# Kernel tuning notes

Measured on AMD Instinct MI355X. Metric: run time of the kernel, lower is better.

The kernel has to match this reference:

```python
import jax, jax.numpy as jnp
import numpy as np

H, W = 64, 64
B, P, F = 8, 512, 512
EXPAND = 0.02      # bbox expansion for soft silhouette (NDC units), DIB-R default
MULT = 1000.0      # DIB-R coordinate multiplier
DELTA = 7000.0     # soft prob falloff in multiplier-scaled squared units, DIB-R default
EPS = 1e-10


def setup_inputs() -> dict:
    key = jax.random.key(0)
    k1, k2, k3 = jax.random.split(key, 3)
    verts = 0.5 * jax.random.normal(k1, (B, P, 3), dtype=jnp.float32)
    faces = jax.random.randint(k2, (B, F, 3), 0, P, dtype=jnp.int32)
    colors = jax.random.uniform(k3, (B, P, 3), dtype=jnp.float32)
    camera_rot = jnp.tile(jnp.eye(3, dtype=jnp.float32)[None], (B, 1, 1))
    camera_pos = jnp.tile(jnp.array([0.0, 0.0, 3.0], dtype=jnp.float32)[None], (B, 1))
    fov_factor = 2.7475  # 1 / tan(fovy/2), fovy ~ 0.7 rad, aspect 1
    camera_proj = jnp.array([[fov_factor], [fov_factor], [-1.0]], dtype=jnp.float32)
    return {"verts": verts, "faces": faces, "camera_rot": camera_rot,
            "camera_pos": camera_pos, "camera_proj": camera_proj, "colors": colors}


def _render_one(verts_p3, faces_f3, rot_33, pos_3, proj_31, colors_p3):
    # --- perspective_projection (pixel2mesh convention: p' = rot^T (p - pos)) ---
    pcam = (verts_p3 - pos_3[None, :]) @ rot_33.T                 # [P,3] camera frame
    xy3 = pcam * proj_31.reshape(3)[None, :]
    xy = xy3[:, :2] / xy3[:, 2:3]                                  # [P,2] NDC
    tri3d = pcam[faces_f3]                                         # [F,3,3]
    tri2d = xy[faces_f3]                                           # [F,3,2]
    normal = jnp.cross(tri3d[:, 1] - tri3d[:, 0], tri3d[:, 2] - tri3d[:, 0])  # [F,3]
    normalz = normal[:, 2]
    normal1 = normal / (jnp.linalg.norm(normal, axis=1, keepdims=True) + 1e-12)
    # per-face vertex colors + hard-mask channel -> [F,3,4] (== color_1xfx12)
    cmask = jnp.ones((faces_f3.shape[0], 3, 1), dtype=colors_p3.dtype)
    cfeat = jnp.concatenate([colors_p3[faces_f3], cmask], axis=2)

    # --- linear_rasterizer: pixel grid in NDC ---
    xs = (2.0 * jnp.arange(W, dtype=jnp.float32) + 1.0 - W) / W
    ys = (H - 2.0 * jnp.arange(H, dtype=jnp.float32) - 1.0) / H
    x0 = xs[None, :, None]                                         # [1,W,1]
    y0 = ys[:, None, None]                                         # [H,1,1]
    ax, ay = tri2d[:, 0, 0], tri2d[:, 0, 1]
    bx, by = tri2d[:, 1, 0], tri2d[:, 1, 1]
    cx, cy = tri2d[:, 2, 0], tri2d[:, 2, 1]
    det = (by - cy) * (ax - cx) + (cx - bx) * (ay - cy)            # [F]
    det_safe = jnp.where(jnp.abs(det) < EPS, EPS, det)
    w0 = ((by - cy) * (x0 - cx) + (cx - bx) * (y0 - cy)) / det_safe  # [H,W,F]
    w1 = ((cy - ay) * (x0 - cx) + (ax - cx) * (y0 - cy)) / det_safe
    w2 = 1.0 - w0 - w1
    z = w0 * tri3d[:, 0, 2] + w1 * tri3d[:, 1, 2] + w2 * tri3d[:, 2, 2]  # [H,W,F]
    covered = (w0 >= 0) & (w1 >= 0) & (w2 >= 0)
    valid = covered & (normalz > 0) & (jnp.abs(det) > EPS)
    # hard z-buffer: camera looks along -z, so nearest face has max z
    zbuf = jnp.where(valid, z, -1e10)
    best = jnp.argmax(zbuf, axis=-1)                               # [H,W]
    anyv = jnp.any(valid, axis=-1)
    gw = lambda w: jnp.take_along_axis(w, best[..., None], axis=-1)[..., 0]
    g0, g1, g2 = gw(w0), gw(w1), gw(w2)
    cb = cfeat[best]                                               # [H,W,3,4]
    feat = (g0[..., None] * cb[..., 0, :] + g1[..., None] * cb[..., 1, :]
            + g2[..., None] * cb[..., 2, :])
    imfeat = jnp.where(anyv[..., None], feat, 0.0)                 # [H,W,4]

    # --- soft silhouette probability ---
    def seg_d2(px, py, qx, qy):
        vx, vy = qx - px, qy - py
        t = jnp.clip(((x0 - px) * vx + (y0 - py) * vy)
                     / (vx * vx + vy * vy + 1e-12), 0.0, 1.0)
        dx, dy = x0 - (px + t * vx), y0 - (py + t * vy)
        return dx * dx + dy * dy
    d2 = jnp.minimum(jnp.minimum(seg_d2(ax, ay, bx, by), seg_d2(bx, by, cx, cy)),
                     seg_d2(cx, cy, ax, ay))
    d2 = jnp.where(covered, 0.0, d2)                               # inside -> 0
    xmin = jnp.minimum(jnp.minimum(ax, bx), cx) - EXPAND
    xmax = jnp.maximum(jnp.maximum(ax, bx), cx) + EXPAND
    ymin = jnp.minimum(jnp.minimum(ay, by), cy) - EXPAND
    ymax = jnp.maximum(jnp.maximum(ay, by), cy) + EXPAND
    in_bbox = (x0 >= xmin) & (x0 <= xmax) & (y0 >= ymin) & (y0 <= ymax)
    contrib = jnp.where(in_bbox, jnp.exp(-d2 * (MULT * MULT) / DELTA), 0.0)
    improb = 1.0 - jnp.prod(1.0 - contrib, axis=-1, keepdims=True)  # [H,W,1]
    return imfeat, improb, normal1


def reference(verts, faces, camera_rot, camera_pos, camera_proj, colors):
    imfeat, improb, normal1 = jax.vmap(_render_one, in_axes=(0, 0, 0, 0, None, 0))(
        verts, faces, camera_rot, camera_pos, camera_proj, colors)
    imrender = imfeat[..., :3]     # [B,H,W,3]
    hardmask = imfeat[..., 3:]     # [B,H,W,1]
    return imrender, improb, normal1, hardmask
```

## Files before the change

### kernel.cpp

```cpp
#include <hip/hip_runtime.h>
#include <math.h>

#define NB 8
#define NP 512
#define NF 512
#define NH 64
#define NW 64
#define FEXPAND 0.02f
#define FEPS 1e-10f

#define IMG_OFF 0
#define PROB_OFF (NB*NH*NW*3)
#define NRM_OFF  (PROB_OFF + NB*NH*NW)
#define MASK_OFF (NRM_OFF + NB*NF*3)

__device__ __forceinline__ void bary(float e0x, float e0y, float e1x, float e1y,
                                     float det_safe, float cx, float cy,
                                     float x, float y,
                                     float& w0, float& w1, float& w2,
                                     float& dxc, float& dyc) {
  dxc = x - cx; dyc = y - cy;
  float n0 = __fadd_rn(__fmul_rn(e0x, dxc), __fmul_rn(e0y, dyc));
  float n1 = __fadd_rn(__fmul_rn(e1x, dxc), __fmul_rn(e1y, dyc));
  w0 = __fdiv_rn(n0, det_safe);
  w1 = __fdiv_rn(n1, det_safe);
  w2 = __fsub_rn(__fsub_rn(1.0f, w0), w1);
}

__global__ __launch_bounds__(1024, 8) void render_all(
    const float* __restrict__ verts, const int* __restrict__ faces,
    const float* __restrict__ rot, const float* __restrict__ pos,
    const float* __restrict__ proj, const float* __restrict__ colors,
    float* __restrict__ out)
{
  __shared__ __align__(16) float smem[NF*20];
  int tid  = threadIdx.x;
  int b    = blockIdx.x >> 6;
  int tile = blockIdx.x & 63;
  int wave = tid >> 6;
  int lane = tid & 63;
  int ix = (tile & 7)*8 + (lane & 7);
  int iy = (tile >> 3)*8 + (lane >> 3);
  float x = (2.0f*ix + 1.0f - 64.0f) * (1.0f/64.0f);
  float y = (64.0f - 2.0f*iy - 1.0f) * (1.0f/64.0f);

  if (tid < NF) {
    int t = b * NF + tid;
    float p0 = proj[0], p1 = proj[1], p2 = proj[2];
    float R0=rot[b*9+0],R1=rot[b*9+1],R2=rot[b*9+2];
    float R3=rot[b*9+3],R4=rot[b*9+4],R5=rot[b*9+5];
    float R6=rot[b*9+6],R7=rot[b*9+7],R8=rot[b*9+8];
    float ppx=pos[b*3+0], ppy=pos[b*3+1], ppz=pos[b*3+2];
    int idxs[3] = { faces[t*3+0], faces[t*3+1], faces[t*3+2] };
    float X[3],Y[3],Z[3],SX[3],SY[3];
#pragma unroll
    for (int k = 0; k < 3; ++k) {
      const float* v = verts + ((size_t)b*NP + idxs[k])*3;
      float dx = v[0]-ppx, dy = v[1]-ppy, dz = v[2]-ppz;
      float pcx = __fadd_rn(__fadd_rn(__fmul_rn(R0,dx),__fmul_rn(R1,dy)),__fmul_rn(R2,dz));
      float pcy = __fadd_rn(__fadd_rn(__fmul_rn(R3,dx),__fmul_rn(R4,dy)),__fmul_rn(R5,dz));
      float pcz = __fadd_rn(__fadd_rn(__fmul_rn(R6,dx),__fmul_rn(R7,dy)),__fmul_rn(R8,dz));
      X[k]=pcx; Y[k]=pcy; Z[k]=pcz;
      float dn = __fmul_rn(pcz, p2);
      SX[k] = __fdiv_rn(__fmul_rn(pcx, p0), dn);
      SY[k] = __fdiv_rn(__fmul_rn(pcy, p1), dn);
    }
    float e1x=X[1]-X[0], e1y=Y[1]-Y[0], e1z=Z[1]-Z[0];
    float e2x=X[2]-X[0], e2y=Y[2]-Y[0], e2z=Z[2]-Z[0];
    float nzel = __fsub_rn(__fmul_rn(e1x,e2y), __fmul_rn(e1y,e2x));
    if (tile == 0) {
      float m0 = __fmul_rn(e1z, e2y); float nxf = __fmaf_rn(e1y, e2z, -m0);
      float m1 = __fmul_rn(e1x, e2z); float nyf = __fmaf_rn(e1z, e2x, -m1);
      float m2 = __fmul_rn(e1y, e2x); float nzf = __fmaf_rn(e1x, e2y, -m2);
      float nn = __fsqrt_rn(__fadd_rn(__fadd_rn(__fmul_rn(nxf,nxf),__fmul_rn(nyf,nyf)),
                                      __fmul_rn(nzf,nzf)));
      float den = __fadd_rn(nn, 1e-12f);
      out[NRM_OFF + (size_t)t*3+0] = __fdiv_rn(nxf, den);
      out[NRM_OFF + (size_t)t*3+1] = __fdiv_rn(nyf, den);
      out[NRM_OFF + (size_t)t*3+2] = __fdiv_rn(nzf, den);
    }
    float ax=SX[0],ay=SY[0],bx=SX[1],by=SY[1],cx=SX[2],cy=SY[2];
    float det = __fadd_rn(__fmul_rn(__fsub_rn(by,cy),__fsub_rn(ax,cx)),
                          __fmul_rn(__fsub_rn(cx,bx),__fsub_rn(ay,cy)));
    float det_safe = (fabsf(det) < FEPS) ? FEPS : det;
    float validf = ((nzel > 0.0f) && (fabsf(det) > FEPS)) ? 1.0f : 0.0f;
    float* d = &smem[tid*20];
    d[0]=ax; d[1]=ay; d[2]=bx; d[3]=by;
    d[4]=cx; d[5]=cy; d[6]=det_safe; d[7]=validf;
    d[8]=Z[0]; d[9]=Z[1]; d[10]=Z[2];
    float vx=bx-ax, vy=by-ay;
    d[11]=1.0f/(vx*vx+vy*vy+1e-12f);
    d[12]=fminf(fminf(ax,bx),cx)-FEXPAND; d[13]=fmaxf(fmaxf(ax,bx),cx)+FEXPAND;
    d[14]=fminf(fminf(ay,by),cy)-FEXPAND; d[15]=fmaxf(fmaxf(ay,by),cy)+FEXPAND;
    vx=cx-bx; vy=cy-by;
    d[16]=1.0f/(vx*vx+vy*vy+1e-12f);
    vx=ax-cx; vy=ay-cy;
    d[17]=1.0f/(vx*vx+vy*vy+1e-12f);
    d[18]=0.0f; d[19]=0.0f;
  }
  __syncthreads();

  float bestz = -1e10f;
  int   bestf = 0;
  float bw0 = 0.0f, bw1 = 0.0f, bw2 = 0.0f;
  float prod  = 1.0f;

  float4 bb = *(const float4*)&smem[wave*20 + 12];
  for (int j = 0; j < 32; ++j) {
    int f = (j << 4) + wave;
    float4 bbn = bb;
    if (j < 31) bbn = *(const float4*)&smem[(f + 16)*20 + 12];
    bool inb = (x >= bb.x) && (x <= bb.y) && (y >= bb.z) && (y <= bb.w);
    if (__any(inb)) {
      const float* r = &smem[f*20];
      float4 q0 = *(const float4*)(r);
      float4 q1 = *(const float4*)(r + 4);
      float4 q2 = *(const float4*)(r + 8);
      float iBC = r[16], iCA = r[17];
      float ax=q0.x, ay=q0.y, bxx=q0.z, byy=q0.w, cx=q1.x, cy=q1.y;
      float e0x=__fsub_rn(byy,cy), e0y=__fsub_rn(cx,bxx);
      float e1x=__fsub_rn(cy,ay),  e1y=__fsub_rn(ax,cx);
      float w0,w1,w2,dxc,dyc;
      bary(e0x,e0y,e1x,e1y, q1.z, cx, cy, x, y, w0,w1,w2,dxc,dyc);
      bool covered = (w0 >= 0.0f) && (w1 >= 0.0f) && (w2 >= 0.0f);
      bool valid   = covered && (q1.w > 0.5f);
      float z = __fadd_rn(__fadd_rn(__fmul_rn(w0,q2.x), __fmul_rn(w1,q2.y)),
                          __fmul_rn(w2,q2.z));
      if (inb) {
        float zval = valid ? z : -1e10f;
        if (zval > bestz) { bestz = zval; bestf = f; bw0 = w0; bw1 = w1; bw2 = w2; }
        float dxa = x - ax, dya = y - ay;
        float vABx=__fsub_rn(bxx,ax), vABy=__fsub_rn(byy,ay);
        float t1 = fminf(fmaxf((dxa*vABx + dya*vABy)*q2.w, 0.0f), 1.0f);
        float rx = dxa - t1*vABx, ry = dya - t1*vABy;
        float d2 = rx*rx + ry*ry;
        float dxb = x - bxx, dyb = y - byy;
        float vBCx=__fsub_rn(cx,bxx), vBCy=__fsub_rn(cy,byy);
        t1 = fminf(fmaxf((dxb*vBCx + dyb*vBCy)*iBC, 0.0f), 1.0f);
        rx = dxb - t1*vBCx; ry = dyb - t1*vBCy;
        d2 = fminf(d2, rx*rx + ry*ry);
        float vCAx=__fsub_rn(ax,cx), vCAy=__fsub_rn(ay,cy);
        t1 = fminf(fmaxf((dxc*vCAx + dyc*vCAy)*iCA, 0.0f), 1.0f);
        rx = dxc - t1*vCAx; ry = dyc - t1*vCAy;
        d2 = fminf(d2, rx*rx + ry*ry);
        d2 = covered ? 0.0f : d2;
        prod *= (1.0f - __expf(d2 * -142.85714285714286f));
      }
    }
    bb = bbn;
  }

  __syncthreads();
  float* comb = smem;
  float* c = comb + (size_t)(wave*64 + lane)*7;
  c[0]=bestz; c[1]=__int_as_float(bestf); c[2]=prod;
  c[3]=bw0; c[4]=bw1; c[5]=bw2;
  __syncthreads();

  if (tid < 64) {
    const float* c0 = comb + (size_t)tid*7;
    float bz = c0[0]; int bf = __float_as_int(c0[1]); float pr = c0[2];
    float w0 = c0[3], w1 = c0[4], w2 = c0[5];
    for (int s = 1; s < 16; ++s) {
      const float* cs = comb + (size_t)(s*64 + tid)*7;
      float oz = cs[0]; int of = __float_as_int(cs[1]);
      if (oz > bz || (oz == bz && of < bf)) { bz = oz; bf = of; w0 = cs[3]; w1 = cs[4]; w2 = cs[5]; }
      pr *= cs[2];
    }
    int av = (bz != -1e10f);
    int t = b * NF + bf;
    const int* fi = faces + (size_t)t*3;
    const float* cb = colors + (size_t)b*NP*3;
    int i0 = fi[0], i1 = fi[1], i2 = fi[2];
    float fr  = w0*cb[i0*3+0] + w1*cb[i1*3+0] + w2*cb[i2*3+0];
    float fgc = w0*cb[i0*3+1] + w1*cb[i1*3+1] + w2*cb[i2*3+1];
    float fb  = w0*cb[i0*3+2] + w1*cb[i1*3+2] + w2*cb[i2*3+2];
    float fa  = __fadd_rn(__fadd_rn(w0, w1), w2);
    int gp = b*4096 + iy*64 + ix;
    out[IMG_OFF + (size_t)gp*3 + 0] = av ? fr  : 0.0f;
    out[IMG_OFF + (size_t)gp*3 + 1] = av ? fgc : 0.0f;
    out[IMG_OFF + (size_t)gp*3 + 2] = av ? fb  : 0.0f;
    out[PROB_OFF + gp] = 1.0f - pr;
    out[MASK_OFF + gp] = av ? fa : 0.0f;
  }
}

extern "C" void kernel_launch(void* const* d_in, const int* in_sizes, int n_in,
                              void* d_out, int out_size, void* d_ws, size_t ws_size,
                              hipStream_t stream) {
  const float* verts  = (const float*)d_in[0];
  const int*   faces  = (const int*)  d_in[1];
  const float* rot    = (const float*)d_in[2];
  const float* pos    = (const float*)d_in[3];
  const float* proj   = (const float*)d_in[4];
  const float* colors = (const float*)d_in[5];
  float* out = (float*)d_out;
  (void)d_ws; (void)ws_size;

  hipLaunchKernelGGL(render_all, dim3(NB*64), dim3(1024), 0, stream,
                     verts, faces, rot, pos, proj, colors, out);
}
```

Baseline: 94.09 us.

## Precompute edge vectors and skip division and distance work via sign tests

The per-face shared record grows from 20 to 32 floats and now holds precomputed edge and segment vectors. The inner loop tests barycentric signs against the sign of the determinant before doing any division. The divides and depth test run only when some lane is both inside the bbox and passing that test. Once a pixel is covered its soft product is set to zero and later segment-distance work is skipped for it. This trades larger shared memory use and more wave-level branches for fewer divides and exp calls per pixel-face pair.

```diff
diff --git a/kernel.cpp b/kernel.cpp
--- a/kernel.cpp
+++ b/kernel.cpp
@@ -14,26 +14,13 @@
 #define NRM_OFF  (PROB_OFF + NB*NH*NW)
 #define MASK_OFF (NRM_OFF + NB*NF*3)
 
-__device__ __forceinline__ void bary(float e0x, float e0y, float e1x, float e1y,
-                                     float det_safe, float cx, float cy,
-                                     float x, float y,
-                                     float& w0, float& w1, float& w2,
-                                     float& dxc, float& dyc) {
-  dxc = x - cx; dyc = y - cy;
-  float n0 = __fadd_rn(__fmul_rn(e0x, dxc), __fmul_rn(e0y, dyc));
-  float n1 = __fadd_rn(__fmul_rn(e1x, dxc), __fmul_rn(e1y, dyc));
-  w0 = __fdiv_rn(n0, det_safe);
-  w1 = __fdiv_rn(n1, det_safe);
-  w2 = __fsub_rn(__fsub_rn(1.0f, w0), w1);
-}
-
 __global__ __launch_bounds__(1024, 8) void render_all(
     const float* __restrict__ verts, const int* __restrict__ faces,
     const float* __restrict__ rot, const float* __restrict__ pos,
     const float* __restrict__ proj, const float* __restrict__ colors,
     float* __restrict__ out)
 {
-  __shared__ __align__(16) float smem[NF*20];
+  __shared__ __align__(16) float smem[NF*32];
   int tid  = threadIdx.x;
   int b    = blockIdx.x >> 6;
   int tile = blockIdx.x & 63;
@@ -84,19 +71,22 @@
                           __fmul_rn(__fsub_rn(cx,bx),__fsub_rn(ay,cy)));
     float det_safe = (fabsf(det) < FEPS) ? FEPS : det;
     float validf = ((nzel > 0.0f) && (fabsf(det) > FEPS)) ? 1.0f : 0.0f;
-    float* d = &smem[tid*20];
-    d[0]=ax; d[1]=ay; d[2]=bx; d[3]=by;
+    float* d = &smem[tid*32];
+    d[0]=__fsub_rn(by,cy); d[1]=__fsub_rn(cx,bx);
+    d[2]=__fsub_rn(cy,ay); d[3]=__fsub_rn(ax,cx);
     d[4]=cx; d[5]=cy; d[6]=det_safe; d[7]=validf;
     d[8]=Z[0]; d[9]=Z[1]; d[10]=Z[2];
     float vx=bx-ax, vy=by-ay;
     d[11]=1.0f/(vx*vx+vy*vy+1e-12f);
+    d[20]=vx; d[21]=vy;
     d[12]=fminf(fminf(ax,bx),cx)-FEXPAND; d[13]=fmaxf(fmaxf(ax,bx),cx)+FEXPAND;
     d[14]=fminf(fminf(ay,by),cy)-FEXPAND; d[15]=fmaxf(fmaxf(ay,by),cy)+FEXPAND;
+    d[16]=ax; d[17]=ay; d[18]=bx; d[19]=by;
     vx=cx-bx; vy=cy-by;
-    d[16]=1.0f/(vx*vx+vy*vy+1e-12f);
+    d[22]=vx; d[23]=vy; d[26]=1.0f/(vx*vx+vy*vy+1e-12f);
     vx=ax-cx; vy=ay-cy;
-    d[17]=1.0f/(vx*vx+vy*vy+1e-12f);
-    d[18]=0.0f; d[19]=0.0f;
+    d[24]=vx; d[25]=vy; d[27]=1.0f/(vx*vx+vy*vy+1e-12f);
+    d[28]=0.0f; d[29]=0.0f; d[30]=0.0f; d[31]=0.0f;
   }
   __syncthreads();
 
@@ -105,46 +95,56 @@
   float bw0 = 0.0f, bw1 = 0.0f, bw2 = 0.0f;
   float prod  = 1.0f;
 
-  float4 bb = *(const float4*)&smem[wave*20 + 12];
+  float4 bb = *(const float4*)&smem[wave*32 + 12];
   for (int j = 0; j < 32; ++j) {
     int f = (j << 4) + wave;
     float4 bbn = bb;
-    if (j < 31) bbn = *(const float4*)&smem[(f + 16)*20 + 12];
+    if (j < 31) bbn = *(const float4*)&smem[(f + 16)*32 + 12];
     bool inb = (x >= bb.x) && (x <= bb.y) && (y >= bb.z) && (y <= bb.w);
     if (__any(inb)) {
-      const float* r = &smem[f*20];
-      float4 q0 = *(const float4*)(r);
+      const float* r = &smem[f*32];
+      float4 qe = *(const float4*)(r);
       float4 q1 = *(const float4*)(r + 4);
-      float4 q2 = *(const float4*)(r + 8);
-      float iBC = r[16], iCA = r[17];
-      float ax=q0.x, ay=q0.y, bxx=q0.z, byy=q0.w, cx=q1.x, cy=q1.y;
-      float e0x=__fsub_rn(byy,cy), e0y=__fsub_rn(cx,bxx);
-      float e1x=__fsub_rn(cy,ay),  e1y=__fsub_rn(ax,cx);
-      float w0,w1,w2,dxc,dyc;
-      bary(e0x,e0y,e1x,e1y, q1.z, cx, cy, x, y, w0,w1,w2,dxc,dyc);
-      bool covered = (w0 >= 0.0f) && (w1 >= 0.0f) && (w2 >= 0.0f);
-      bool valid   = covered && (q1.w > 0.5f);
-      float z = __fadd_rn(__fadd_rn(__fmul_rn(w0,q2.x), __fmul_rn(w1,q2.y)),
-                          __fmul_rn(w2,q2.z));
-      if (inb) {
+      float dxc = x - q1.x, dyc = y - q1.y;
+      float n0 = __fadd_rn(__fmul_rn(qe.x, dxc), __fmul_rn(qe.y, dyc));
+      float n1 = __fadd_rn(__fmul_rn(qe.z, dxc), __fmul_rn(qe.w, dyc));
+      bool dsp  = q1.z > 0.0f;
+      bool pass = ((n0 == 0.0f) || ((n0 > 0.0f) == dsp)) &&
+                  ((n1 == 0.0f) || ((n1 > 0.0f) == dsp));
+      bool act = inb && pass;
+      bool covered = false;
+      if (__any(act)) {
+        float4 q2 = *(const float4*)(r + 8);
+        float w0 = __fdiv_rn(n0, q1.z);
+        float w1 = __fdiv_rn(n1, q1.z);
+        float w2 = __fsub_rn(__fsub_rn(1.0f, w0), w1);
+        covered = act && (w2 >= 0.0f);
+        bool valid = covered && (q1.w > 0.5f);
+        float z = __fadd_rn(__fadd_rn(__fmul_rn(w0,q2.x), __fmul_rn(w1,q2.y)),
+                            __fmul_rn(w2,q2.z));
         float zval = valid ? z : -1e10f;
         if (zval > bestz) { bestz = zval; bestf = f; bw0 = w0; bw1 = w1; bw2 = w2; }
-        float dxa = x - ax, dya = y - ay;
-        float vABx=__fsub_rn(bxx,ax), vABy=__fsub_rn(byy,ay);
-        float t1 = fminf(fmaxf((dxa*vABx + dya*vABy)*q2.w, 0.0f), 1.0f);
-        float rx = dxa - t1*vABx, ry = dya - t1*vABy;
+      }
+      if (covered) prod = 0.0f;
+      bool needd = inb && !covered && (prod != 0.0f);
+      if (__any(needd)) {
+        float4 qa = *(const float4*)(r + 16);
+        float4 qv = *(const float4*)(r + 20);
+        float4 qw = *(const float4*)(r + 24);
+        float invAB = r[11];
+        float dxa = x - qa.x, dya = y - qa.y;
+        float t1 = fminf(fmaxf((dxa*qv.x + dya*qv.y)*invAB, 0.0f), 1.0f);
+        float rx = dxa - t1*qv.x, ry = dya - t1*qv.y;
         float d2 = rx*rx + ry*ry;
-        float dxb = x - bxx, dyb = y - byy;
-        float vBCx=__fsub_rn(cx,bxx), vBCy=__fsub_rn(cy,byy);
-        t1 = fminf(fmaxf((dxb*vBCx + dyb*vBCy)*iBC, 0.0f), 1.0f);
-        rx = dxb - t1*vBCx; ry = dyb - t1*vBCy;
+        float dxb = x - qa.z, dyb = y - qa.w;
+        t1 = fminf(fmaxf((dxb*qv.z + dyb*qv.w)*qw.z, 0.0f), 1.0f);
+        rx = dxb - t1*qv.z; ry = dyb - t1*qv.w;
         d2 = fminf(d2, rx*rx + ry*ry);
-        float vCAx=__fsub_rn(ax,cx), vCAy=__fsub_rn(ay,cy);
-        t1 = fminf(fmaxf((dxc*vCAx + dyc*vCAy)*iCA, 0.0f), 1.0f);
-        rx = dxc - t1*vCAx; ry = dyc - t1*vCAy;
+        t1 = fminf(fmaxf((dxc*qw.x + dyc*qw.y)*qw.w, 0.0f), 1.0f);
+        rx = dxc - t1*qw.x; ry = dyc - t1*qw.y;
         d2 = fminf(d2, rx*rx + ry*ry);
-        d2 = covered ? 0.0f : d2;
-        prod *= (1.0f - __expf(d2 * -142.85714285714286f));
+        if (needd)
+          prod *= (1.0f - __expf(d2 * -142.85714285714286f));
       }
     }
     bb = bbn;
```

Measured after the change: 92.05 us. 2.2% less time.
